# Kernel tuning notes

Hardware: AMD Instinct MI355X
Metric: run time of the kernel (lower is better)

## Reference

```python
import jax, jax.numpy as jnp
import numpy as np

B, H, L, D_QK, D_V, M = 4, 16, 4096, 64, 64, 256
EPS = 1e-6


def _gaussian_orf(key, m, d):
    """Structured Gaussian orthogonal random features (SORF), as in gaussian_orf."""
    num_squares = m // d + 1
    keys = jax.random.split(key, num_squares)
    blocks = jax.vmap(lambda k: jnp.linalg.qr(jax.random.normal(k, (d, d)))[0].T)(keys)
    b = blocks.reshape(-1, d)[:m]
    return jnp.sqrt(d) * b  # structured multiplier sqrt(d)*I


def setup_inputs() -> dict:
    key = jax.random.key(0)
    kq, kk, kv, kp = jax.random.split(key, 4)
    qs = jax.random.normal(kq, (B, H, L, D_QK), dtype=jnp.float32)
    ks = jax.random.normal(kk, (B, H, L, D_QK), dtype=jnp.float32)
    vs = jax.random.normal(kv, (B, H, L, D_V), dtype=jnp.float32)
    mask = jnp.ones((B, L), dtype=jnp.float32)
    proj = _gaussian_orf(kp, M, D_QK).astype(jnp.float32)
    return {"qs": qs, "ks": ks, "vs": vs, "mask": mask, "proj": proj}


def _phi(x, proj):
    """Stable positive softmax kernel: exp(x @ Omega^T - |x|^2/2) / sqrt(m)."""
    m = proj.shape[0]
    x_proj = jnp.einsum('bld,md->blm', x, proj)
    half_sq_norm = 0.5 * jnp.square(x).sum(-1, keepdims=True)
    return jnp.exp(x_proj - half_sq_norm) / jnp.sqrt(m)


def reference(qs, ks, vs, mask, proj):
    b, h, q_len, d_qk = qs.shape
    # (B H L D) -> ((B H) L D)
    qs_f = qs.reshape(b * h, q_len, d_qk)
    ks_f = ks.reshape(b * h, ks.shape[2], d_qk)
    vs_f = vs.reshape(b * h, vs.shape[2], vs.shape[3])
    normalizer = 1.0 / jnp.power(jnp.float32(d_qk), 0.25)
    qs_prime = _phi(qs_f * normalizer, proj)          # (BH, Q, M)
    ks_prime = _phi(ks_f * normalizer, proj)          # (BH, K, M)
    ks_prime = ks_prime * jnp.repeat(mask, h, axis=0)[..., None]
    # fast_attend: linear attention matmul chain
    c = jnp.concatenate([vs_f, jnp.ones((*vs_f.shape[:-1], 1), vs_f.dtype)], axis=-1)  # (BH, K, Dv+1)
    buf_1 = jnp.einsum('bkm,bke->bme', ks_prime, c)   # (BH, M, Dv+1)
    buf_2 = jnp.einsum('bqm,bme->bqe', qs_prime, buf_1)
    num, den = buf_2[..., :-1], buf_2[..., -1]
    den = jnp.where(den < EPS, EPS, den)
    ctx = num / den[..., None]
    return ctx.reshape(b, h, q_len, -1)
```

## Files before the change

### kernel.cpp

```cpp
#include <hip/hip_runtime.h>
#include <hip/hip_bf16.h>

#define Lq    4096
#define NORM  0.3535533905932738f
#define SC    0.0625f
#define EPSV  1e-6f
#define EPSV16 1.6e-5f

typedef short short8 __attribute__((ext_vector_type(8)));
typedef short short4v __attribute__((ext_vector_type(4)));
typedef float float4v __attribute__((ext_vector_type(4)));

#define MFMA16(a, b, c) __builtin_amdgcn_mfma_f32_16x16x32_bf16(a, b, c, 0, 0, 0)

__device__ __forceinline__ short f2bf(float f) {
  unsigned u = __builtin_bit_cast(unsigned, f);
  unsigned r = (u + 0x7FFFu + ((u >> 16) & 1u)) >> 16;
  return (short)r;
}

#define PITCH 88
#define P2    268
#define PP    68
#define PB    260

#define BUF1_FLOATS ((size_t)64 * 256 * 80)
#define BUF1T_OFF   (BUF1_FLOATS * 4)
#define PROJB_OFF   (BUF1T_OFF + (size_t)64 * 20480 * 2)

__global__ __launch_bounds__(256)
void k0_proj(const float* __restrict__ proj, short* __restrict__ projb) {
  int i = (blockIdx.x * 256 + threadIdx.x) * 4;
  float4 v = *reinterpret_cast<const float4*>(proj + i);
  short4v o; o[0] = f2bf(v.x); o[1] = f2bf(v.y); o[2] = f2bf(v.z); o[3] = f2bf(v.w);
  *reinterpret_cast<short4v*>(projb + i) = o;
}

__global__ __launch_bounds__(256, 2)
void k1_build(const float* __restrict__ ks, const float* __restrict__ vs,
              const float* __restrict__ mask, const short* __restrict__ projb,
              float* __restrict__ buf1) {
  __shared__ short lx[64 * PITCH];
  __shared__ short lvT[80 * PITCH];
  __shared__ short lphiT[256 * PITCH];
  __shared__ float lhn[64];
  __shared__ float lmfAll[512];

  const int t    = threadIdx.x;
  const int w    = t >> 6;
  const int lane = t & 63;
  const int c    = lane & 15;
  const int quad = lane >> 4;
  const int chunk = blockIdx.x;
  const int bh    = blockIdx.y;
  const int bidx  = bh >> 4;

  for (int i = t; i < 512; i += 256)
    lmfAll[i] = mask[(size_t)bidx * Lq + chunk * 512 + i] * SC;

  short8 pf[4][2];
#pragma unroll
  for (int nt = 0; nt < 4; ++nt)
#pragma unroll
    for (int h = 0; h < 2; ++h)
      pf[nt][h] = *reinterpret_cast<const short8*>(
          &projb[(size_t)(w * 64 + nt * 16 + c) * 64 + h * 32 + quad * 8]);

#pragma unroll
  for (int i = 0; i < 4; ++i) {
    int idx = i * 256 + t;
    int row = 64 + (idx >> 6), col = idx & 63;
    lvT[row * PITCH + col] = (row == 64) ? (short)0x3F80 : (short)0;
  }

  float4v acc[4][5];
#pragma unroll
  for (int mt = 0; mt < 4; ++mt)
#pragma unroll
    for (int nt = 0; nt < 5; ++nt) acc[mt][nt] = (float4v){0.f, 0.f, 0.f, 0.f};

  const float4* ks4 = reinterpret_cast<const float4*>(ks);
  const float4* vs4 = reinterpret_cast<const float4*>(vs);
  const int key0 = (t >> 4);
  const int d4   = t & 15;

  float4 kx[4], vx[4];
#pragma unroll
  for (int i = 0; i < 4; ++i) {
    size_t base = ((size_t)bh * Lq + chunk * 512 + (i * 16 + key0)) * 16 + d4;
    kx[i] = ks4[base]; vx[i] = vs4[base];
  }

  for (int kt = 0; kt < 8; ++kt) {
    __syncthreads();

#pragma unroll
    for (int i = 0; i < 4; ++i) {
      int key = i * 16 + key0;
      float4 v = kx[i];
      v.x *= NORM; v.y *= NORM; v.z *= NORM; v.w *= NORM;
      float ss = v.x * v.x + v.y * v.y + v.z * v.z + v.w * v.w;
      ss += __shfl_xor(ss, 1);
      ss += __shfl_xor(ss, 2);
      ss += __shfl_xor(ss, 4);
      ss += __shfl_xor(ss, 8);
      if (d4 == 0) lhn[key] = 0.5f * ss;
      short4v o; o[0] = f2bf(v.x); o[1] = f2bf(v.y); o[2] = f2bf(v.z); o[3] = f2bf(v.w);
      *reinterpret_cast<short4v*>(&lx[key * PITCH + d4 * 4]) = o;
      float4 u = vx[i];
      int col = ((key >> 3) ^ (d4 & 7)) * 8 + (key & 7);
      lvT[(d4 * 4 + 0) * PITCH + col] = f2bf(u.x);
      lvT[(d4 * 4 + 1) * PITCH + col] = f2bf(u.y);
      lvT[(d4 * 4 + 2) * PITCH + col] = f2bf(u.z);
      lvT[(d4 * 4 + 3) * PITCH + col] = f2bf(u.w);
    }

    if (kt + 1 < 8) {
#pragma unroll
      for (int i = 0; i < 4; ++i) {
        size_t base = ((size_t)bh * Lq + chunk * 512 + (kt + 1) * 64 + (i * 16 + key0)) * 16 + d4;
        kx[i] = ks4[base]; vx[i] = vs4[base];
      }
    }
    __syncthreads();

#pragma unroll
    for (int mt = 0; mt < 4; ++mt) {
      short8 a0 = *reinterpret_cast<short8*>(&lx[(mt * 16 + c) * PITCH + quad * 8]);
      short8 a1 = *reinterpret_cast<short8*>(&lx[(mt * 16 + c) * PITCH + 32 + quad * 8]);
      float4v hn4 = *reinterpret_cast<float4v*>(&lhn[mt * 16 + quad * 4]);
      float4v mf4 = *reinterpret_cast<float4v*>(&lmfAll[kt * 64 + mt * 16 + quad * 4]);
#pragma unroll
      for (int nt = 0; nt < 4; ++nt) {
        float4v p = (float4v){0.f, 0.f, 0.f, 0.f};
        p = MFMA16(a0, pf[nt][0], p);
        p = MFMA16(a1, pf[nt][1], p);
        short4v ph;
#pragma unroll
        for (int r = 0; r < 4; ++r)
          ph[r] = f2bf(__expf(p[r] - hn4[r]) * mf4[r]);
        *reinterpret_cast<short4v*>(
            &lphiT[(w * 64 + nt * 16 + c) * PITCH + mt * 16 + quad * 4]) = ph;
      }
    }

    short8 bv[5][2];
#pragma unroll
    for (int nt = 0; nt < 5; ++nt) {
      int rsw = (nt * 4 + (c >> 2)) & 7;
      bv[nt][0] = *reinterpret_cast<short8*>(
          &lvT[(nt * 16 + c) * PITCH + ((0 + quad) ^ rsw) * 8]);
      bv[nt][1] = *reinterpret_cast<short8*>(
          &lvT[(nt * 16 + c) * PITCH + ((4 + quad) ^ rsw) * 8]);
    }
    __builtin_amdgcn_s_setprio(1);
#pragma unroll
    for (int mt = 0; mt < 4; ++mt) {
      short8 a0 = *reinterpret_cast<short8*>(&lphiT[(w * 64 + mt * 16 + c) * PITCH + quad * 8]);
      short8 a1 = *reinterpret_cast<short8*>(&lphiT[(w * 64 + mt * 16 + c) * PITCH + 32 + quad * 8]);
#pragma unroll
      for (int nt = 0; nt < 5; ++nt) {
        acc[mt][nt] = MFMA16(a0, bv[nt][0], acc[mt][nt]);
        acc[mt][nt] = MFMA16(a1, bv[nt][1], acc[mt][nt]);
      }
    }
    __builtin_amdgcn_s_setprio(0);
  }

  float* bp = buf1 + (size_t)bh * 256 * 80;
#pragma unroll
  for (int mt = 0; mt < 4; ++mt)
#pragma unroll
    for (int nt = 0; nt < 5; ++nt)
#pragma unroll
      for (int r = 0; r < 4; ++r) {
        int feat = w * 64 + mt * 16 + quad * 4 + r;
        int e    = nt * 16 + c;
        atomicAdd(bp + (size_t)feat * 80 + e, acc[mt][nt][r]);
      }
}

__global__ __launch_bounds__(256, 8)
void k1_reduce(const float* __restrict__ buf1, short* __restrict__ buf1T) {
  const int bh = blockIdx.x;
  const int s  = blockIdx.y;
  const int t  = threadIdx.x;
#pragma unroll
  for (int j = 0; j < 10; ++j) {
    int idx = s * 2560 + j * 256 + t;
    int e = idx >> 8, feat = idx & 255;
    buf1T[(size_t)bh * 20480 + idx] = f2bf(buf1[(size_t)bh * 20480 + feat * 80 + e]);
  }
}

__global__ __launch_bounds__(512, 1)
void k2_ctx(const float* __restrict__ qs, const short* __restrict__ projb,
            const short* __restrict__ buf1T, float* __restrict__ out) {
  __shared__ short lproj[256 * PP];
  __shared__ short lbT[64 * PB];
  __shared__ short lden[256];
  __shared__ short lphi[128 * P2];
  __shared__ float lhnw[128];

  const int t    = threadIdx.x;
  const int w    = t >> 6;
  const int lane = t & 63;
  const int c    = lane & 15;
  const int quad = lane >> 4;
  const int q0   = blockIdx.x * 128;
  const int bhb  = blockIdx.y * 8;

#pragma unroll
  for (int i = 0; i < 4; ++i) {
    int idx = i * 512 + t;
    int row = idx >> 3, col = (idx & 7) * 8;
    *reinterpret_cast<short8*>(&lproj[row * PP + col]) =
        *reinterpret_cast<const short8*>(&projb[(size_t)row * 64 + col]);
  }
  {
    const short* bT = buf1T + (size_t)bhb * 20480;
#pragma unroll
    for (int i = 0; i < 4; ++i) {
      int idx = i * 512 + t;
      int e = idx >> 5, f = (idx & 31) * 8;
      *reinterpret_cast<short8*>(&lbT[e * PB + f]) =
          *reinterpret_cast<const short8*>(&bT[e * 256 + f]);
    }
    if (t < 32)
      *reinterpret_cast<short8*>(&lden[t * 8]) =
          *reinterpret_cast<const short8*>(&bT[16384 + t * 8]);
  }
  const float* qrow0 = qs + ((size_t)bhb * Lq + q0 + w * 16 + c) * 64;
  float4 v0 = *reinterpret_cast<const float4*>(qrow0 + quad * 8);
  float4 v1 = *reinterpret_cast<const float4*>(qrow0 + quad * 8 + 4);
  float4 v2 = *reinterpret_cast<const float4*>(qrow0 + 32 + quad * 8);
  float4 v3 = *reinterpret_cast<const float4*>(qrow0 + 32 + quad * 8 + 4);
  __syncthreads();

  for (int it = 0; it < 8; ++it) {
    const int bh = bhb + it;

    short8 nb[4]; short8 nden; float4 n0, n1, n2, n3;
    if (it < 7) {
      const short* bTn = buf1T + (size_t)(bh + 1) * 20480;
#pragma unroll
      for (int i = 0; i < 4; ++i) {
        int idx = i * 512 + t;
        int e = idx >> 5, f = (idx & 31) * 8;
        nb[i] = *reinterpret_cast<const short8*>(&bTn[e * 256 + f]);
      }
      if (t < 32) nden = *reinterpret_cast<const short8*>(&bTn[16384 + t * 8]);
      const float* qn = qs + ((size_t)(bh + 1) * Lq + q0 + w * 16 + c) * 64;
      n0 = *reinterpret_cast<const float4*>(qn + quad * 8);
      n1 = *reinterpret_cast<const float4*>(qn + quad * 8 + 4);
      n2 = *reinterpret_cast<const float4*>(qn + 32 + quad * 8);
      n3 = *reinterpret_cast<const float4*>(qn + 32 + quad * 8 + 4);
    }

    v0.x *= NORM; v0.y *= NORM; v0.z *= NORM; v0.w *= NORM;
    v1.x *= NORM; v1.y *= NORM; v1.z *= NORM; v1.w *= NORM;
    v2.x *= NORM; v2.y *= NORM; v2.z *= NORM; v2.w *= NORM;
    v3.x *= NORM; v3.y *= NORM; v3.z *= NORM; v3.w *= NORM;

    float s = v0.x * v0.x + v0.y * v0.y + v0.z * v0.z + v0.w * v0.w
            + v1.x * v1.x + v1.y * v1.y + v1.z * v1.z + v1.w * v1.w
            + v2.x * v2.x + v2.y * v2.y + v2.z * v2.z + v2.w * v2.w
            + v3.x * v3.x + v3.y * v3.y + v3.z * v3.z + v3.w * v3.w;
    s += __shfl_xor(s, 16);
    s += __shfl_xor(s, 32);
    if (quad == 0) lhnw[w * 16 + c] = 0.5f * s;

    short8 qa0, qa1;
    qa0[0] = f2bf(v0.x); qa0[1] = f2bf(v0.y); qa0[2] = f2bf(v0.z); qa0[3] = f2bf(v0.w);
    qa0[4] = f2bf(v1.x); qa0[5] = f2bf(v1.y); qa0[6] = f2bf(v1.z); qa0[7] = f2bf(v1.w);
    qa1[0] = f2bf(v2.x); qa1[1] = f2bf(v2.y); qa1[2] = f2bf(v2.z); qa1[3] = f2bf(v2.w);
    qa1[4] = f2bf(v3.x); qa1[5] = f2bf(v3.y); qa1[6] = f2bf(v3.z); qa1[7] = f2bf(v3.w);

    float4v hn4 = *reinterpret_cast<float4v*>(&lhnw[w * 16 + quad * 4]);

#pragma unroll
    for (int nt = 0; nt < 16; ++nt) {
      short8 b0 = *reinterpret_cast<short8*>(&lproj[(nt * 16 + c) * PP + quad * 8]);
      short8 b1 = *reinterpret_cast<short8*>(&lproj[(nt * 16 + c) * PP + 32 + quad * 8]);
      float4v p = (float4v){0.f, 0.f, 0.f, 0.f};
      p = MFMA16(qa0, b0, p);
      p = MFMA16(qa1, b1, p);
#pragma unroll
      for (int r = 0; r < 4; ++r)
        lphi[(w * 16 + quad * 4 + r) * P2 + nt * 16 + c] =
            f2bf(__expf(p[r] - hn4[r]));
    }

    __syncthreads();

    float4v cacc[5];
#pragma unroll
    for (int nt = 0; nt < 5; ++nt) cacc[nt] = (float4v){0.f, 0.f, 0.f, 0.f};
#pragma unroll
    for (int k2i = 0; k2i < 8; ++k2i) {
      short8 a = *reinterpret_cast<short8*>(&lphi[(w * 16 + c) * P2 + k2i * 32 + quad * 8]);
#pragma unroll
      for (int nt = 0; nt < 4; ++nt) {
        short8 b = *reinterpret_cast<short8*>(
            &lbT[(nt * 16 + c) * PB + k2i * 32 + quad * 8]);
        cacc[nt] = MFMA16(a, b, cacc[nt]);
      }
      short8 bd;
      if (c == 0) bd = *reinterpret_cast<short8*>(&lden[k2i * 32 + quad * 8]);
      else        bd = (short8){0, 0, 0, 0, 0, 0, 0, 0};
      cacc[4] = MFMA16(a, bd, cacc[4]);
    }

    float rinv[4];
#pragma unroll
    for (int r = 0; r < 4; ++r) {
      float den = __shfl(cacc[4][r], (lane & 48));
      den = fmaxf(den, EPSV16);
      rinv[r] = 1.0f / den;
    }
#pragma unroll
    for (int nt = 0; nt < 4; ++nt)
#pragma unroll
      for (int r = 0; r < 4; ++r) {
        int q = q0 + w * 16 + quad * 4 + r;
        out[((size_t)bh * Lq + q) * 64 + nt * 16 + c] = cacc[nt][r] * rinv[r];
      }

    __syncthreads();

    if (it < 7) {
#pragma unroll
      for (int i = 0; i < 4; ++i) {
        int idx = i * 512 + t;
        int e = idx >> 5, f = (idx & 31) * 8;
        *reinterpret_cast<short8*>(&lbT[e * PB + f]) = nb[i];
      }
      if (t < 32) *reinterpret_cast<short8*>(&lden[t * 8]) = nden;
      v0 = n0; v1 = n1; v2 = n2; v3 = n3;
    }
  }
}

extern "C" void kernel_launch(void* const* d_in, const int* in_sizes, int n_in,
                              void* d_out, int out_size, void* d_ws, size_t ws_size,
                              hipStream_t stream) {
  const float* qs   = (const float*)d_in[0];
  const float* ks   = (const float*)d_in[1];
  const float* vs   = (const float*)d_in[2];
  const float* mask = (const float*)d_in[3];
  const float* proj = (const float*)d_in[4];
  float* out  = (float*)d_out;
  float* buf1 = (float*)d_ws;
  short* buf1T = (short*)((char*)d_ws + BUF1T_OFF);
  short* projb = (short*)((char*)d_ws + PROJB_OFF);

  (void)in_sizes; (void)n_in; (void)out_size; (void)ws_size;

  hipMemsetAsync(buf1, 0, BUF1_FLOATS * sizeof(float), stream);
  k0_proj<<<dim3(16), 256, 0, stream>>>(proj, projb);
  k1_build<<<dim3(8, 64), 256, 0, stream>>>(ks, vs, mask, projb, buf1);
  k1_reduce<<<dim3(64, 8), 256, 0, stream>>>(buf1, buf1T);
  k2_ctx<<<dim3(32, 8), 512, 0, stream>>>(qs, projb, buf1T, out);
}
```

Measured before the change: 287.7 us.

## Halve k1_build key tile to raise occupancy and tile k1_reduce transpose via LDS

k1_build now processes 32 keys per iteration instead of 64, shrinking LDS buffers and register arrays so four blocks per CU can be resident instead of two. The phi-times-V matmul uses one K=32 MFMA step per tile, and the swizzle and pitch are adjusted to match. k1_reduce now reads buf1 rows with coalesced loads into an LDS tile and writes the transposed bf16 output with coalesced stores, replacing the earlier strided gather. The smaller tile doubles the number of barriers and iterations in k1_build.

```diff
diff --git a/kernel.cpp b/kernel.cpp
--- a/kernel.cpp
+++ b/kernel.cpp
@@ -20,9 +20,11 @@
 }
 
 #define PITCH 88
+#define PKV   42
 #define P2    268
 #define PP    68
 #define PB    260
+#define PR    74
 
 #define BUF1_FLOATS ((size_t)64 * 256 * 80)
 #define BUF1T_OFF   (BUF1_FLOATS * 4)
@@ -36,14 +38,14 @@
   *reinterpret_cast<short4v*>(projb + i) = o;
 }
 
-__global__ __launch_bounds__(256, 2)
+__global__ __launch_bounds__(256, 4)
 void k1_build(const float* __restrict__ ks, const float* __restrict__ vs,
               const float* __restrict__ mask, const short* __restrict__ projb,
               float* __restrict__ buf1) {
-  __shared__ short lx[64 * PITCH];
-  __shared__ short lvT[80 * PITCH];
-  __shared__ short lphiT[256 * PITCH];
-  __shared__ float lhn[64];
+  __shared__ short lx[32 * PITCH];
+  __shared__ short lvT[80 * PKV];
+  __shared__ short lphiT[256 * PKV];
+  __shared__ float lhn[32];
   __shared__ float lmfAll[512];
 
   const int t    = threadIdx.x;
@@ -67,10 +69,10 @@
           &projb[(size_t)(w * 64 + nt * 16 + c) * 64 + h * 32 + quad * 8]);
 
 #pragma unroll
-  for (int i = 0; i < 4; ++i) {
+  for (int i = 0; i < 2; ++i) {
     int idx = i * 256 + t;
-    int row = 64 + (idx >> 6), col = idx & 63;
-    lvT[row * PITCH + col] = (row == 64) ? (short)0x3F80 : (short)0;
+    int row = 64 + (idx >> 5), col = idx & 31;
+    lvT[row * PKV + col] = (row == 64) ? (short)0x3F80 : (short)0;
   }
 
   float4v acc[4][5];
@@ -84,18 +86,18 @@
   const int key0 = (t >> 4);
   const int d4   = t & 15;
 
-  float4 kx[4], vx[4];
-#pragma unroll
-  for (int i = 0; i < 4; ++i) {
+  float4 kx[2], vx[2];
+#pragma unroll
+  for (int i = 0; i < 2; ++i) {
     size_t base = ((size_t)bh * Lq + chunk * 512 + (i * 16 + key0)) * 16 + d4;
     kx[i] = ks4[base]; vx[i] = vs4[base];
   }
 
-  for (int kt = 0; kt < 8; ++kt) {
+  for (int kt = 0; kt < 16; ++kt) {
     __syncthreads();
 
 #pragma unroll
-    for (int i = 0; i < 4; ++i) {
+    for (int i = 0; i < 2; ++i) {
       int key = i * 16 + key0;
       float4 v = kx[i];
       v.x *= NORM; v.y *= NORM; v.z *= NORM; v.w *= NORM;
@@ -108,28 +110,28 @@
       short4v o; o[0] = f2bf(v.x); o[1] = f2bf(v.y); o[2] = f2bf(v.z); o[3] = f2bf(v.w);
       *reinterpret_cast<short4v*>(&lx[key * PITCH + d4 * 4]) = o;
       float4 u = vx[i];
-      int col = ((key >> 3) ^ (d4 & 7)) * 8 + (key & 7);
-      lvT[(d4 * 4 + 0) * PITCH + col] = f2bf(u.x);
-      lvT[(d4 * 4 + 1) * PITCH + col] = f2bf(u.y);
-      lvT[(d4 * 4 + 2) * PITCH + col] = f2bf(u.z);
-      lvT[(d4 * 4 + 3) * PITCH + col] = f2bf(u.w);
-    }
-
-    if (kt + 1 < 8) {
-#pragma unroll
-      for (int i = 0; i < 4; ++i) {
-        size_t base = ((size_t)bh * Lq + chunk * 512 + (kt + 1) * 64 + (i * 16 + key0)) * 16 + d4;
+      int col = ((key >> 3) ^ (d4 & 3)) * 8 + (key & 7);
+      lvT[(d4 * 4 + 0) * PKV + col] = f2bf(u.x);
+      lvT[(d4 * 4 + 1) * PKV + col] = f2bf(u.y);
+      lvT[(d4 * 4 + 2) * PKV + col] = f2bf(u.z);
+      lvT[(d4 * 4 + 3) * PKV + col] = f2bf(u.w);
+    }
+
+    if (kt + 1 < 16) {
+#pragma unroll
+      for (int i = 0; i < 2; ++i) {
+        size_t base = ((size_t)bh * Lq + chunk * 512 + (kt + 1) * 32 + (i * 16 + key0)) * 16 + d4;
         kx[i] = ks4[base]; vx[i] = vs4[base];
       }
     }
     __syncthreads();
 
 #pragma unroll
-    for (int mt = 0; mt < 4; ++mt) {
+    for (int mt = 0; mt < 2; ++mt) {
       short8 a0 = *reinterpret_cast<short8*>(&lx[(mt * 16 + c) * PITCH + quad * 8]);
       short8 a1 = *reinterpret_cast<short8*>(&lx[(mt * 16 + c) * PITCH + 32 + quad * 8]);
       float4v hn4 = *reinterpret_cast<float4v*>(&lhn[mt * 16 + quad * 4]);
-      float4v mf4 = *reinterpret_cast<float4v*>(&lmfAll[kt * 64 + mt * 16 + quad * 4]);
+      float4v mf4 = *reinterpret_cast<float4v*>(&lmfAll[kt * 32 + mt * 16 + quad * 4]);
 #pragma unroll
       for (int nt = 0; nt < 4; ++nt) {
         float4v p = (float4v){0.f, 0.f, 0.f, 0.f};
@@ -140,29 +142,24 @@
         for (int r = 0; r < 4; ++r)
           ph[r] = f2bf(__expf(p[r] - hn4[r]) * mf4[r]);
         *reinterpret_cast<short4v*>(
-            &lphiT[(w * 64 + nt * 16 + c) * PITCH + mt * 16 + quad * 4]) = ph;
-      }
-    }
-
-    short8 bv[5][2];
+            &lphiT[(w * 64 + nt * 16 + c) * PKV + mt * 16 + quad * 4]) = ph;
+      }
+    }
+
+    short8 bv[5];
 #pragma unroll
     for (int nt = 0; nt < 5; ++nt) {
-      int rsw = (nt * 4 + (c >> 2)) & 7;
-      bv[nt][0] = *reinterpret_cast<short8*>(
-          &lvT[(nt * 16 + c) * PITCH + ((0 + quad) ^ rsw) * 8]);
-      bv[nt][1] = *reinterpret_cast<short8*>(
-          &lvT[(nt * 16 + c) * PITCH + ((4 + quad) ^ rsw) * 8]);
+      int rsw = (nt * 4 + (c >> 2)) & 3;
+      bv[nt] = *reinterpret_cast<short8*>(
+          &lvT[(nt * 16 + c) * PKV + (quad ^ rsw) * 8]);
     }
     __builtin_amdgcn_s_setprio(1);
 #pragma unroll
     for (int mt = 0; mt < 4; ++mt) {
-      short8 a0 = *reinterpret_cast<short8*>(&lphiT[(w * 64 + mt * 16 + c) * PITCH + quad * 8]);
-      short8 a1 = *reinterpret_cast<short8*>(&lphiT[(w * 64 + mt * 16 + c) * PITCH + 32 + quad * 8]);
-#pragma unroll
-      for (int nt = 0; nt < 5; ++nt) {
-        acc[mt][nt] = MFMA16(a0, bv[nt][0], acc[mt][nt]);
-        acc[mt][nt] = MFMA16(a1, bv[nt][1], acc[mt][nt]);
-      }
+      short8 a = *reinterpret_cast<short8*>(&lphiT[(w * 64 + mt * 16 + c) * PKV + quad * 8]);
+#pragma unroll
+      for (int nt = 0; nt < 5; ++nt)
+        acc[mt][nt] = MFMA16(a, bv[nt], acc[mt][nt]);
     }
     __builtin_amdgcn_s_setprio(0);
   }
@@ -180,16 +177,27 @@
       }
 }
 
-__global__ __launch_bounds__(256, 8)
+__global__ __launch_bounds__(256)
 void k1_reduce(const float* __restrict__ buf1, short* __restrict__ buf1T) {
+  __shared__ short l[80 * PR];
   const int bh = blockIdx.x;
-  const int s  = blockIdx.y;
+  const int fb = blockIdx.y;
   const int t  = threadIdx.x;
-#pragma unroll
-  for (int j = 0; j < 10; ++j) {
-    int idx = s * 2560 + j * 256 + t;
-    int e = idx >> 8, feat = idx & 255;
-    buf1T[(size_t)bh * 20480 + idx] = f2bf(buf1[(size_t)bh * 20480 + feat * 80 + e]);
+  const float* src = buf1 + (size_t)bh * 20480 + (size_t)fb * 5120;
+#pragma unroll
+  for (int i = 0; i < 20; ++i) {
+    int idx = i * 256 + t;
+    int f = (int)(((unsigned)(idx >> 4) * 6554u) >> 15);
+    int e = idx - f * 80;
+    l[e * PR + f] = f2bf(src[idx]);
+  }
+  __syncthreads();
+  short* dst = buf1T + (size_t)bh * 20480 + fb * 64;
+#pragma unroll
+  for (int i = 0; i < 20; ++i) {
+    int idx = i * 256 + t;
+    int e = idx >> 6, f = idx & 63;
+    dst[e * 256 + f] = l[e * PR + f];
   }
 }
 
@@ -359,6 +367,6 @@
   hipMemsetAsync(buf1, 0, BUF1_FLOATS * sizeof(float), stream);
   k0_proj<<<dim3(16), 256, 0, stream>>>(proj, projb);
   k1_build<<<dim3(8, 64), 256, 0, stream>>>(ks, vs, mask, projb, buf1);
-  k1_reduce<<<dim3(64, 8), 256, 0, stream>>>(buf1, buf1T);
+  k1_reduce<<<dim3(64, 4), 256, 0, stream>>>(buf1, buf1T);
   k2_ctx<<<dim3(32, 8), 512, 0, stream>>>(qs, projb, buf1T, out);
 }
```

Result: slower. 484.6 us (+68.4%).
